# Performance work log

Hardware: AMD Instinct MI355X
Metric: run time of the kernel (lower is better)

Reference implementation:

```python
import jax, jax.numpy as jnp
import numpy as np
import math

D, NS, PP, POS = 256, 4, 4, 16
PI = math.pi
LN_EPS = 1e-5


def _gelu(x):
    return jax.nn.gelu(x, approximate=False)  # torch default GELU is exact erf


def _mlp(x, W1, b1, W2, b2):
    return _gelu(x @ W1 + b1) @ W2 + b2


def setup_inputs() -> dict:
    key = jax.random.key(0)
    ks = jax.random.split(key, 16)

    def lin(k, fi, fo):
        k1, k2 = jax.random.split(k)
        s = 1.0 / np.sqrt(fi)
        W = jax.random.uniform(k1, (fi, fo), minval=-s, maxval=s, dtype=jnp.float32)
        b = jax.random.uniform(k2, (fo,), minval=-s, maxval=s, dtype=jnp.float32)
        return W, b

    x = jax.random.normal(ks[0], (2, 2048, D), dtype=jnp.float32)
    kW1, kb1 = lin(ks[1], D, D); kW2, kb2 = lin(ks[2], D, NS * PP)
    qW1, qb1 = lin(ks[3], D, D); qW2, qb2 = lin(ks[4], D, NS * PP)
    vW, vb = lin(ks[5], D, D)
    oW, ob = lin(ks[6], D, D)
    gW1, gb1 = lin(ks[7], D, D // 2); gW2, gb2 = lin(ks[8], D // 2, 1)
    lW1, lb1 = lin(ks[9], D, D); lW2, lb2 = lin(ks[10], D, POS)
    lvW, lvb = lin(ks[11], D, D)
    pos_freqs = jnp.exp(jnp.arange(POS, dtype=jnp.float32) * (-math.log(10000.0) / POS))
    return dict(
        x=x, kW1=kW1, kb1=kb1, kW2=kW2, kb2=kb2,
        qW1=qW1, qb1=qb1, qW2=qW2, qb2=qb2, vW=vW, vb=vb,
        ln_g=jnp.ones((D,), jnp.float32), ln_b=jnp.zeros((D,), jnp.float32), oW=oW, ob=ob,
        set_weights=jnp.ones((NS,), jnp.float32), pos_freqs=pos_freqs,
        pos_weight=jnp.ones((1,), jnp.float32),
        gW1=gW1, gb1=gb1, gW2=gW2, gb2=gb2,
        lW1=lW1, lb1=lb1, lW2=lW2, lb2=lb2, lvW=lvW, lvb=lvb,
        surprise_scale=jnp.float32(1.0), surprise_bias=jnp.float32(0.0),
        ltm_weight=jnp.float32(0.5),
    )


def _fwd(x, kW1, kb1, kW2, kb2, qW1, qb1, qW2, qb2, vW, vb, ln_g, ln_b, oW, ob,
         set_weights, pos_freqs, pos_weight, gW1, gb1, gW2, gb2,
         lW1, lb1, lW2, lb2, lvW, lvb, surprise_scale, surprise_bias, ltm_weight):
    B, L, Dd = x.shape
    key_phasor = jnp.exp(1j * (jnp.tanh(_mlp(x, kW1, kb1, kW2, kb2)) * PI)).reshape(B, L, NS, PP)
    query_phasor = jnp.exp(1j * (jnp.tanh(_mlp(x, qW1, qb1, qW2, qb2)) * PI)).reshape(B, L, NS, PP)
    V_real = x @ vW + vb  # (B,L,D)
    weights = jax.nn.softmax(set_weights)

    pos_cb = jnp.maximum(jnp.arange(L, dtype=jnp.float32), 1.0)  # shifted positions, clamp(min=1)

    # ---- cross-bank (joint product over sets) + surprise write gate ----
    joint_key = jnp.prod(key_phasor, axis=2)    # (B,L,PP)
    joint_query = jnp.prod(query_phasor, axis=2)
    km_shift = jnp.concatenate(
        [jnp.zeros_like(joint_key[:, :1]), jnp.cumsum(joint_key[:, :-1], axis=1)], axis=1)
    res_mag = jnp.abs((km_shift * jnp.conj(joint_key)).sum(-1))  # (B,L)
    familiarity = jnp.clip(res_mag / (pos_cb * math.sqrt(PP)), 0.0, 1.0)[..., None]
    write_gate = jax.nn.sigmoid(surprise_scale * ((1.0 - familiarity) - 0.5) + surprise_bias)
    V_gated = (V_real * write_gate).astype(jnp.complex64)

    bound = joint_key[..., None] * V_gated[:, :, None, :]       # (B,L,PP,D)
    memory = jnp.cumsum(bound, axis=1)
    cross_bank = (memory * jnp.conj(joint_query)[..., None]).sum(2).real  # (B,L,D)

    # ---- per-bank binding/retrieval ----
    bound_all = key_phasor[..., None] * V_gated[:, :, None, None, :]  # (B,L,NS,PP,D)
    mem_all = jnp.cumsum(bound_all, axis=1)
    retr_per_bank = (mem_all * jnp.conj(query_phasor)[..., None]).sum(3).real  # (B,L,NS,D)
    total = (retr_per_bank * weights[None, None, :, None]).sum(2)
    total = (total + cross_bank) / (NS + 1)

    # ---- positional phasor bank ----
    V = V_real.astype(jnp.complex64)
    pos_phasor = jnp.exp(1j * (jnp.arange(L, dtype=jnp.float32)[:, None] * pos_freqs * 2 * PI))  # (L,POS)
    bound_pos = pos_phasor[None, :, :, None] * V[:, :, None, :]  # (B,L,POS,D)
    mem_pos = jnp.cumsum(bound_pos, axis=1)
    retr_pos = (mem_pos * jnp.conj(pos_phasor)[None, :, :, None]).sum(2).real
    gate = jax.nn.sigmoid(_mlp(x, gW1, gb1, gW2, gb2))  # (B,L,1)
    total = gate * total + (1 - gate) * (jax.nn.sigmoid(pos_weight) * retr_pos)

    # ---- LTM bank with surprise gating ----
    ltm_kp = jnp.exp(1j * (jnp.tanh(_mlp(x, lW1, lb1, lW2, lb2)) * PI))  # (B,L,POS)
    ltm_val = x @ lvW + lvb
    km2 = jnp.concatenate(
        [jnp.zeros_like(ltm_kp[:, :1]), jnp.cumsum(ltm_kp[:, :-1], axis=1)], axis=1)
    res2 = jnp.abs((km2 * jnp.conj(ltm_kp)).sum(-1))
    fam2 = jnp.clip(res2 / (pos_cb * math.sqrt(POS)), 0.0, 1.0)[..., None]
    wg2 = jax.nn.sigmoid(surprise_scale * ((1.0 - fam2) - 0.5) + surprise_bias)  # (B,L,1)
    gated_bind = wg2[:, :, None, :] * ltm_kp[..., None] * ltm_val.astype(jnp.complex64)[:, :, None, :]
    ltm_mem = jnp.cumsum(gated_bind, axis=1)                      # (B,L,POS,D)
    ltm_retr = (ltm_mem * jnp.conj(ltm_kp)[..., None]).sum(2).real
    pos1 = jnp.arange(1, L + 1, dtype=jnp.float32)
    ltm_retr = ltm_retr / jnp.sqrt(pos1 * POS)[None, :, None]
    total = total + jax.nn.sigmoid(ltm_weight) * ltm_retr

    # ---- output projection: LayerNorm + Linear, residual ----
    t = total / jnp.sqrt(pos1 * PP)[None, :, None]
    mu = t.mean(-1, keepdims=True)
    var = t.var(-1, keepdims=True)
    tn = (t - mu) / jnp.sqrt(var + LN_EPS) * ln_g + ln_b
    return x + tn @ oW + ob


def reference(x, kW1, kb1, kW2, kb2, qW1, qb1, qW2, qb2, vW, vb, ln_g, ln_b, oW, ob,
              set_weights, pos_freqs, pos_weight, gW1, gb1, gW2, gb2,
              lW1, lb1, lW2, lb2, lvW, lvb, surprise_scale, surprise_bias, ltm_weight):
    return _fwd(x, kW1, kb1, kW2, kb2, qW1, qb1, qW2, qb2, vW, vb, ln_g, ln_b, oW, ob,
                set_weights, pos_freqs, pos_weight, gW1, gb1, gW2, gb2,
                lW1, lb1, lW2, lb2, lvW, lvb, surprise_scale, surprise_bias, ltm_weight)
```

## Files before the change

### kernel.cpp

```cpp
#include <hip/hip_runtime.h>
#include <math.h>

#define DD   256
#define NSB  4
#define PPB  4
#define POSB 16
#define LL   2048
#define BB   2
#define NC   32
#define CHK  64
#define NG   13
#define FS   128
#define PI_F 3.14159265358979323846f

#define JK_OFF   0
#define JQ_OFF   8
#define KP_OFF   16
#define QP_OFF   48
#define LKP_OFF  80
#define GATE_OFF 112

#define FEAT_O  0L
#define V_O     524288L
#define LV_O    1572864L
#define PPH_O   2621440L
#define TOT_O   2686976L
#define CMEM_O  3735552L
#define WGB_O   5439488L
#define WS_FLOATS 5447680L
#define KM_O    CMEM_O
#define XH_O    CMEM_O
#define XL_O    (CMEM_O + 524288L)
#define WTH_O   (CMEM_O + 1048576L)
#define WT2H_O  (CMEM_O + 1245184L)

typedef __attribute__((ext_vector_type(8))) short bf16x8;
typedef __attribute__((ext_vector_type(4))) float f32x4;

__device__ __forceinline__ float sigm(float v){ return 1.0f/(1.0f+expf(-v)); }
__device__ __forceinline__ float gelu_exact(float v){ return 0.5f*v*(1.0f+erff(v*0.70710678118654752f)); }
__device__ __forceinline__ unsigned short f2bf(float f){
    unsigned u = __float_as_uint(f);
    unsigned r = u + 0x7fffu + ((u>>16)&1u);
    return (unsigned short)(r>>16);
}
__device__ __forceinline__ float bf2f(unsigned short h){ return __uint_as_float(((unsigned)h)<<16); }

__global__ __launch_bounds__(256) void prep_all(
    const float* __restrict__ x,
    const float* __restrict__ kW1, const float* __restrict__ qW1, const float* __restrict__ lW1,
    const float* __restrict__ vW,  const float* __restrict__ lvW, const float* __restrict__ gW1,
    const float* __restrict__ kW2, const float* __restrict__ qW2, const float* __restrict__ lW2,
    const float* __restrict__ pf,
    unsigned short* __restrict__ xh, unsigned short* __restrict__ xl,
    unsigned short* __restrict__ wth, unsigned short* __restrict__ wt2h,
    float* __restrict__ posph)
{
    int bid = blockIdx.x, tid = threadIdx.x;
    if (bid < 512){
        int gid = bid*256 + tid;
        int frag = gid>>6, lane = gid&63;
        int tile = frag>>3, ksb = frag&7;
        int row = tile*16 + (lane&15);
        int k0  = ksb*32 + ((lane>>4)&3)*8;
        const float* xp = x + (long)row*DD + k0;
        unsigned short h8[8], l8[8];
        #pragma unroll
        for (int e=0;e<8;++e){
            float f = xp[e];
            unsigned short h = f2bf(f);
            h8[e] = h;
            l8[e] = f2bf(f - bf2f(h));
        }
        *(bf16x8*)(xh + (long)gid*8) = *(bf16x8*)h8;
        *(bf16x8*)(xl + (long)gid*8) = *(bf16x8*)l8;
    } else if (bid < 512+192){
        int gid = (bid-512)*256 + tid;
        int frag = gid>>6, lane = gid&63;
        int tile = frag>>3, ksb = frag&7;
        int col = tile*16 + (lane&15);
        int k0  = ksb*32 + ((lane>>4)&3)*8;
        unsigned short h8[8];
        #pragma unroll
        for (int e=0;e<8;++e){
            int fi = k0 + e;
            float w = 0.f;
            if (col < 1408){
                int m = col >> 8;
                if (m < 5){
                    const float* W = (m==0)?kW1:((m==1)?qW1:((m==2)?lW1:((m==3)?vW:lvW)));
                    w = W[(long)fi*DD + (col & 255)];
                } else {
                    w = gW1[(long)fi*128 + (col - 1280)];
                }
            }
            h8[e] = f2bf(w);
        }
        *(bf16x8*)(wth + (long)gid*8) = *(bf16x8*)h8;
    } else if (bid < 512+192+48){
        int blk = bid - (512+192);
        int m = blk>>4, o = blk&15;
        const float* W2 = (m==0)?kW2:((m==1)?qW2:lW2);
        wt2h[(long)blk*DD + tid] = f2bf(W2[tid*16+o]);
    } else {
        int t = (bid - (512+192+48))*256 + tid;
        if (t < LL){
            #pragma unroll
            for (int j=0;j<POSB;++j){
                float ang = (((float)t * pf[j]) * 2.0f) * PI_F;
                float s,c; sincosf(ang,&s,&c);
                posph[t*32+2*j]   = c;
                posph[t*32+2*j+1] = s;
            }
        }
    }
}

__global__ __launch_bounds__(256) void mlp_fused(
    const unsigned short* __restrict__ xh, const unsigned short* __restrict__ xl,
    const unsigned short* __restrict__ wth, const unsigned short* __restrict__ wt2h,
    const float* __restrict__ kb1, const float* __restrict__ kb2,
    const float* __restrict__ qb1, const float* __restrict__ qb2,
    const float* __restrict__ lb1, const float* __restrict__ lb2,
    const float* __restrict__ vb,  const float* __restrict__ lvb,
    const float* __restrict__ gb1, const float* __restrict__ gW2, const float* __restrict__ gb2,
    float* __restrict__ feat, float* __restrict__ Vbuf, float* __restrict__ lvalbuf)
{
    __shared__ __align__(16) char smraw[18432];
    int tid = threadIdx.x, lane = tid & 63, wv = tid >> 6;
    int mat = blockIdx.x >> 7, bm = blockIdx.x & 127;
    int rowg0 = bm*32;
    int ar = lane & 15, kk = (lane>>4)*8;

    f32x4 acc[2][4];
    #pragma unroll
    for (int i=0;i<2;++i)
        #pragma unroll
        for (int j=0;j<4;++j) acc[i][j] = (f32x4){0.f,0.f,0.f,0.f};

    bf16x8 ah[2], al[2], bh[4];
    {
        #pragma unroll
        for (int i=0;i<2;++i){
            long off = (((long)(2*bm+i)*8 + 0)*64 + lane)*8;
            ah[i] = *reinterpret_cast<const bf16x8*>(xh + off);
            al[i] = *reinterpret_cast<const bf16x8*>(xl + off);
        }
        #pragma unroll
        for (int j=0;j<4;++j){
            long off = (((long)(mat*16 + wv*4 + j)*8 + 0)*64 + lane)*8;
            bh[j] = *reinterpret_cast<const bf16x8*>(wth + off);
        }
    }
    #pragma unroll
    for (int ksb=0; ksb<8; ++ksb){
        bf16x8 nah[2], nal[2], nbh[4];
        if (ksb < 7){
            #pragma unroll
            for (int i=0;i<2;++i){
                long off = (((long)(2*bm+i)*8 + ksb+1)*64 + lane)*8;
                nah[i] = *reinterpret_cast<const bf16x8*>(xh + off);
                nal[i] = *reinterpret_cast<const bf16x8*>(xl + off);
            }
            #pragma unroll
            for (int j=0;j<4;++j){
                long off = (((long)(mat*16 + wv*4 + j)*8 + ksb+1)*64 + lane)*8;
                nbh[j] = *reinterpret_cast<const bf16x8*>(wth + off);
            }
        }
        #pragma unroll
        for (int i=0;i<2;++i)
            #pragma unroll
            for (int j=0;j<4;++j){
                acc[i][j] = __builtin_amdgcn_mfma_f32_16x16x32_bf16(ah[i], bh[j], acc[i][j], 0,0,0);
                acc[i][j] = __builtin_amdgcn_mfma_f32_16x16x32_bf16(al[i], bh[j], acc[i][j], 0,0,0);
            }
        if (ksb < 7){
            #pragma unroll
            for (int i=0;i<2;++i){ ah[i]=nah[i]; al[i]=nal[i]; }
            #pragma unroll
            for (int j=0;j<4;++j) bh[j]=nbh[j];
        }
    }

    int rl0 = (lane>>4)*4;

    if (mat < 3){
        float (*ang)[16] = (float(*)[16])(smraw + 16384);
        const float* b1 = (mat==0)?kb1:((mat==1)?qb1:lb1);
        #pragma unroll
        for (int i=0;i<2;++i)
            #pragma unroll
            for (int j=0;j<4;++j){
                int c = wv*64 + j*16 + ar;
                #pragma unroll
                for (int r=0;r<4;++r){
                    int row = i*16 + rl0 + r;
                    float hv = gelu_exact(acc[i][j][r] + b1[c]);
                    int bo = row*512 + c*2;
                    *(unsigned short*)(smraw + (bo ^ ((row&7)<<4))) = f2bf(hv);
                }
            }
        __syncthreads();
        const float* b2 = (mat==0)?kb2:((mat==1)?qb2:lb2);
        int off = (mat==0)?KP_OFF:((mat==1)?QP_OFF:LKP_OFF);
        if (wv < 2){
            int arow = wv*16 + ar;
            f32x4 a2 = (f32x4){0.f,0.f,0.f,0.f};
            #pragma unroll
            for (int ksb=0; ksb<8; ++ksb){
                int k = ksb*32 + kk;
                int bo = arow*512 + k*2;
                bf16x8 af = *reinterpret_cast<const bf16x8*>(smraw + (bo ^ ((arow&7)<<4)));
                bf16x8 bf = *reinterpret_cast<const bf16x8*>(wt2h + ((long)(mat*16 + ar)*DD + k));
                a2 = __builtin_amdgcn_mfma_f32_16x16x32_bf16(af, bf, a2, 0,0,0);
            }
            int o = ar;
            #pragma unroll
            for (int r=0;r<4;++r){
                int tok = wv*16 + rl0 + r;
                float a = tanhf(a2[r] + b2[o])*PI_F;
                ang[tok][o] = a;
                float sn,cs; sincosf(a,&sn,&cs);
                long rowg = rowg0 + tok;
                feat[rowg*FS + off + 2*o]   = cs;
                feat[rowg*FS + off + 2*o+1] = sn;
            }
        }
        __syncthreads();
        if (mat<2 && tid<128){
            int tok = tid>>2, p = tid&3;
            float a = ang[tok][p]+ang[tok][4+p]+ang[tok][8+p]+ang[tok][12+p];
            float sn,cs; sincosf(a,&sn,&cs);
            int joff = (mat==0)?JK_OFF:JQ_OFF;
            long rowg = rowg0 + tok;
            feat[rowg*FS + joff + 2*p]   = cs;
            feat[rowg*FS + joff + 2*p+1] = sn;
        }
    } else if (mat < 5){
        const float* bv = (mat==3)? vb : lvb;
        float* dst = (mat==3)? Vbuf : lvalbuf;
        #pragma unroll
        for (int i=0;i<2;++i)
            #pragma unroll
            for (int j=0;j<4;++j){
                int c = wv*64 + j*16 + ar;
                #pragma unroll
                for (int r=0;r<4;++r)
                    dst[(long)(rowg0 + i*16 + rl0 + r)*DD + c] = acc[i][j][r] + bv[c];
            }
    } else {
        float (*hg)[132] = (float(*)[132])smraw;
        float (*part)[8] = (float(*)[8])(smraw + 32*132*4);
        if (wv < 2){
            #pragma unroll
            for (int i=0;i<2;++i)
                #pragma unroll
                for (int j=0;j<4;++j){
                    int c = wv*64 + j*16 + ar;
                    #pragma unroll
                    for (int r=0;r<4;++r)
                        hg[i*16 + rl0 + r][c] = gelu_exact(acc[i][j][r] + gb1[c]);
                }
        }
        __syncthreads();
        {
            int tok = tid>>3, jj = tid&7;
            float s = 0.f;
            #pragma unroll
            for (int c=0;c<16;++c) s += hg[tok][jj*16+c]*gW2[jj*16+c];
            part[tok][jj] = s;
        }
        __syncthreads();
        if (tid < 32){
            float s = gb2[0];
            #pragma unroll
            for (int j=0;j<8;++j) s += part[tid][j];
            feat[(long)(rowg0+tid)*FS + GATE_OFF] = sigm(s);
        }
    }
}

__global__ __launch_bounds__(256) void g_prefix(const float* __restrict__ feat, float* __restrict__ km){
    int b = blockIdx.x / 40, ch = blockIdx.x % 40;
    int off = (ch<8) ? (JK_OFF+ch) : (LKP_OFF + (ch-8));
    int tid = threadIdx.x;
    long rb = (long)b*LL*FS;
    float v[8]; float s = 0.f;
    #pragma unroll
    for (int u=0;u<8;++u){
        v[u] = feat[rb + (long)(tid*8+u)*FS + off];
        s += v[u];
    }
    int lane = tid & 63, w = tid >> 6;
    float xsc = s;
    #pragma unroll
    for (int o=1;o<64;o<<=1){ float y = __shfl_up(xsc,o); if (lane>=o) xsc += y; }
    __shared__ float wsum[4];
    if (lane==63) wsum[w] = xsc;
    __syncthreads();
    float woff = 0.f;
    for (int i=0;i<w;++i) woff += wsum[i];
    float run = (xsc - s) + woff;
    #pragma unroll
    for (int u=0;u<8;++u){
        km[((long)b*LL + tid*8+u)*40 + ch] = run;
        run += v[u];
    }
}

__global__ __launch_bounds__(256) void g_fam(
    const float* __restrict__ feat, const float* __restrict__ km,
    const float* __restrict__ ss_p, const float* __restrict__ sb_p,
    float* __restrict__ wgbuf)
{
    int t = blockIdx.x*256 + threadIdx.x;
    if (t >= BB*LL) return;
    int tc = t % LL;
    float ss = ss_p[0], sb = sb_p[0];
    long frow = (long)t*FS;
    const float* kmrow = km + (long)t*40;
    float pcb = fmaxf((float)tc, 1.0f);

    float sr=0.f, si=0.f;
    #pragma unroll
    for (int p=0;p<4;++p){
        float kr = feat[frow+JK_OFF+2*p], ki = feat[frow+JK_OFF+2*p+1];
        float kmr = kmrow[2*p], kmi = kmrow[2*p+1];
        sr += kmr*kr + kmi*ki;
        si += kmi*kr - kmr*ki;
    }
    float res = sqrtf(sr*sr+si*si);
    float fam = fminf(fmaxf(res/(pcb*2.0f),0.f),1.f);
    wgbuf[(long)t*2] = sigm(ss*(0.5f-fam)+sb);

    sr=0.f; si=0.f;
    #pragma unroll
    for (int p=0;p<16;++p){
        float kr = feat[frow+LKP_OFF+2*p], ki = feat[frow+LKP_OFF+2*p+1];
        float kmr = kmrow[8+2*p], kmi = kmrow[8+2*p+1];
        sr += kmr*kr + kmi*ki;
        si += kmi*kr - kmr*ki;
    }
    float res2 = sqrtf(sr*sr+si*si);
    float fam2 = fminf(fmaxf(res2/(pcb*4.0f),0.f),1.f);
    wgbuf[(long)t*2+1] = sigm(ss*(0.5f-fam2)+sb);
}

__global__ __launch_bounds__(128) void m_chunksum(
    const float* __restrict__ feat, const float* __restrict__ posph,
    const float* __restrict__ wgbuf, const float* __restrict__ Vbuf,
    const float* __restrict__ lvalbuf, float* __restrict__ cmem)
{
    int blk = blockIdx.x;
    int dh = blk & 1; blk >>= 1;
    int b = blk/(NG*NC); int r = blk%(NG*NC); int g = r/NC, c = r%NC;
    int d = dh*128 + threadIdx.x;
    __shared__ __align__(16) float4 kl4[CHK][2];
    __shared__ float gl[CHK];
    long frow = ((long)b*LL + c*CHK)*FS;
    for (int idx=threadIdx.x; idx<CHK*2; idx+=128){
        int t = idx>>1, j = idx&1;
        float4 v;
        if (g==0)       v = *(const float4*)&feat[frow + (long)t*FS + JK_OFF + j*4];
        else if (g<5)   v = *(const float4*)&feat[frow + (long)t*FS + KP_OFF + (g-1)*8 + j*4];
        else if (g<9)   v = *(const float4*)&posph[(long)(c*CHK+t)*32 + (g-5)*8 + j*4];
        else            v = *(const float4*)&feat[frow + (long)t*FS + LKP_OFF + (g-9)*8 + j*4];
        kl4[t][j] = v;
    }
    for (int t=threadIdx.x; t<CHK; t+=128){
        float gf;
        if (g<5)      gf = wgbuf[((long)b*LL + c*CHK + t)*2];
        else if (g<9) gf = 1.0f;
        else          gf = wgbuf[((long)b*LL + c*CHK + t)*2 + 1];
        gl[t] = gf;
    }
    __syncthreads();
    const float* vsrc = (g>=9)? lvalbuf : Vbuf;
    long vrow = ((long)b*LL + c*CHK)*DD + d;
    float m0r=0,m0i=0,m1r=0,m1i=0,m2r=0,m2i=0,m3r=0,m3i=0;
    float vnext = vsrc[vrow];
    #pragma unroll 4
    for (int t=0;t<CHK;++t){
        float v = vnext * gl[t];
        if (t+1 < CHK) vnext = vsrc[vrow + (long)(t+1)*DD];
        float4 ka = kl4[t][0], kb = kl4[t][1];
        m0r += ka.x*v; m0i += ka.y*v;
        m1r += ka.z*v; m1i += ka.w*v;
        m2r += kb.x*v; m2i += kb.y*v;
        m3r += kb.z*v; m3i += kb.w*v;
    }
    long grp = (long)((b*NG+g)*NC + c);
    long ob = grp*8*DD + d;
    cmem[ob+0*DD]=m0r; cmem[ob+1*DD]=m0i;
    cmem[ob+2*DD]=m1r; cmem[ob+3*DD]=m1i;
    cmem[ob+4*DD]=m2r; cmem[ob+5*DD]=m2i;
    cmem[ob+6*DD]=m3r; cmem[ob+7*DD]=m3i;
}

__global__ __launch_bounds__(256) void m_scan(float* __restrict__ cmem){
    int line = blockIdx.x;
    int lb = line>>2, slot = line&3, d = threadIdx.x;
    float vr[NC], vi[NC];
    #pragma unroll
    for (int c=0;c<NC;++c){
        long a = (((long)(lb*NC + c)*4 + slot)*2)*DD + d;
        vr[c] = cmem[a]; vi[c] = cmem[a+DD];
    }
    float rr=0.f, ri=0.f;
    #pragma unroll
    for (int c=0;c<NC;++c){
        long a = (((long)(lb*NC + c)*4 + slot)*2)*DD + d;
        cmem[a] = rr; cmem[a+DD] = ri;
        rr += vr[c]; ri += vi[c];
    }
}

__global__ __launch_bounds__(128) void m_retrieve_fam(
    const float* __restrict__ feat, const float* __restrict__ posph,
    const float* __restrict__ wgbuf, const float* __restrict__ Vbuf,
    const float* __restrict__ lvalbuf, const float* __restrict__ cmem,
    const float* __restrict__ set_w, const float* __restrict__ pos_w,
    const float* __restrict__ ltm_w, float* __restrict__ total)
{
    int blk = blockIdx.x;
    int dh = blk & 1; blk >>= 1;
    int b = blk/(3*NC); int r = blk%(3*NC); int fam = r/NC, c = r%NC;
    int d = dh*128 + threadIdx.x;
    __shared__ __align__(16) float4 s_k04[CHK][4];
    __shared__ __align__(16) float4 s_kb4[CHK][8];
    __shared__ __align__(16) float4 s_qb4[CHK][8];
    __shared__ float s_sc[CHK][2];
    long frow = ((long)b*LL + c*CHK)*FS;

    for (int idx=threadIdx.x; idx<CHK*8; idx+=128){
        int t = idx>>3, j = idx&7;
        if (fam==0){
            s_kb4[t][j] = *(const float4*)&feat[frow + (long)t*FS + KP_OFF + j*4];
            s_qb4[t][j] = *(const float4*)&feat[frow + (long)t*FS + QP_OFF + j*4];
        } else if (fam==1){
            s_kb4[t][j] = *(const float4*)&posph[(long)(c*CHK+t)*32 + j*4];
        } else {
            s_kb4[t][j] = *(const float4*)&feat[frow + (long)t*FS + LKP_OFF + j*4];
        }
    }
    if (fam==0){
        for (int idx=threadIdx.x; idx<CHK*4; idx+=128){
            int t = idx>>2, j = idx&3;
            s_k04[t][j] = *(const float4*)&feat[frow + (long)t*FS + JK_OFF + j*4];
        }
    }
    for (int t=threadIdx.x; t<CHK; t+=128){
        int tc = c*CHK + t;
        float gate = feat[frow + (long)t*FS + GATE_OFF];
        if (fam==0){
            s_sc[t][0] = wgbuf[((long)b*LL+tc)*2];
            s_sc[t][1] = gate*0.2f;
        } else if (fam==1){
            s_sc[t][0] = (1.0f-gate)*sigm(pos_w[0]);
            s_sc[t][1] = 0.f;
        } else {
            s_sc[t][0] = wgbuf[((long)b*LL+tc)*2+1];
            s_sc[t][1] = sigm(ltm_w[0]) * rsqrtf((float)(tc+1)*16.0f);
        }
    }
    __syncthreads();

    long vrow = ((long)b*LL + c*CHK)*DD + d;
    float* tp = total + ((long)b*LL + c*CHK)*DD + d;

    if (fam == 0){
        float w0=expf(set_w[0]),w1=expf(set_w[1]),w2=expf(set_w[2]),w3=expf(set_w[3]);
        float den = w0+w1+w2+w3;
        float wn[4] = {w0/den, w1/den, w2/den, w3/den};
        float cr[4], ci[4], br[4][4], bi[4][4];
        #pragma unroll
        for (int s=0;s<4;++s){
            long cb0 = (((long)(b*NG+0)*NC + c)*8 + 2*s)*DD + d;
            cr[s] = cmem[cb0]; ci[s] = cmem[cb0+DD];
        }
        #pragma unroll
        for (int g=0;g<4;++g)
            #pragma unroll
            for (int s=0;s<4;++s){
                long cb = (((long)(b*NG+1+g)*NC + c)*8 + 2*s)*DD + d;
                br[g][s] = cmem[cb]; bi[g][s] = cmem[cb+DD];
            }
        float vnext = Vbuf[vrow];
        #pragma unroll 2
        for (int t=0;t<CHK;++t){
            float v = vnext;
            if (t+1 < CHK) vnext = Vbuf[vrow + (long)(t+1)*DD];
            float vg = v * s_sc[t][0];
            float4 jk0 = s_k04[t][0], jk1 = s_k04[t][1];
            float4 jq0 = s_k04[t][2], jq1 = s_k04[t][3];
            cr[0] += jk0.x*vg; ci[0] += jk0.y*vg;
            cr[1] += jk0.z*vg; ci[1] += jk0.w*vg;
            cr[2] += jk1.x*vg; ci[2] += jk1.y*vg;
            cr[3] += jk1.z*vg; ci[3] += jk1.w*vg;
            float rsc = cr[0]*jq0.x + ci[0]*jq0.y + cr[1]*jq0.z + ci[1]*jq0.w
                      + cr[2]*jq1.x + ci[2]*jq1.y + cr[3]*jq1.z + ci[3]*jq1.w;
            float rbank = 0.f;
            #pragma unroll
            for (int g=0;g<4;++g){
                float4 ka = s_kb4[t][2*g], kb = s_kb4[t][2*g+1];
                float4 qa = s_qb4[t][2*g], qb = s_qb4[t][2*g+1];
                br[g][0] += ka.x*vg; bi[g][0] += ka.y*vg;
                br[g][1] += ka.z*vg; bi[g][1] += ka.w*vg;
                br[g][2] += kb.x*vg; bi[g][2] += kb.y*vg;
                br[g][3] += kb.z*vg; bi[g][3] += kb.w*vg;
                float rg = br[g][0]*qa.x + bi[g][0]*qa.y + br[g][1]*qa.z + bi[g][1]*qa.w
                         + br[g][2]*qb.x + bi[g][2]*qb.y + br[g][3]*qb.z + bi[g][3]*qb.w;
                rbank += rg*wn[g];
            }
            float rs = s_sc[t][1]*(rsc + rbank);
            atomicAdd(tp + (long)t*DD, rs);
        }
    } else {
        const float* vsrc = (fam==2)? lvalbuf : Vbuf;
        int g0 = (fam==1)? 5 : 9;
        float mr[16], mi[16];
        #pragma unroll
        for (int g=0;g<4;++g)
            #pragma unroll
            for (int s=0;s<4;++s){
                long cb = (((long)(b*NG+g0+g)*NC + c)*8 + 2*s)*DD + d;
                mr[g*4+s] = cmem[cb]; mi[g*4+s] = cmem[cb+DD];
            }
        float vnext = vsrc[vrow];
        #pragma unroll 2
        for (int t=0;t<CHK;++t){
            float v = vnext;
            if (t+1 < CHK) vnext = vsrc[vrow + (long)(t+1)*DD];
            float vg = (fam==2)? v*s_sc[t][0] : v;
            float rs = 0.f;
            #pragma unroll
            for (int j=0;j<8;++j){
                float4 ka = s_kb4[t][j];
                mr[2*j]   += ka.x*vg; mi[2*j]   += ka.y*vg;
                rs += mr[2*j]*ka.x + mi[2*j]*ka.y;
                mr[2*j+1] += ka.z*vg; mi[2*j+1] += ka.w*vg;
                rs += mr[2*j+1]*ka.z + mi[2*j+1]*ka.w;
            }
            float sc = (fam==2)? s_sc[t][1] : s_sc[t][0];
            atomicAdd(tp + (long)t*DD, rs*sc);
        }
    }
}

__global__ __launch_bounds__(256) void k4_out(
    const float* __restrict__ x, const float* __restrict__ total,
    const float* __restrict__ ln_g, const float* __restrict__ ln_b,
    const float* __restrict__ oW,  const float* __restrict__ obv,
    float* __restrict__ out)
{
    __shared__ float tn[8][DD];
    int tid = threadIdx.x;
    long base = (long)blockIdx.x*8;
    int wave = tid>>6, lane = tid&63;
    for (int wtok=0; wtok<2; ++wtok){
        int tok = wave*2 + wtok;
        long row = base + tok;
        int tc = (int)(row % LL);
        float inv = rsqrtf((float)(tc+1)*4.0f);
        float4 tv4 = ((const float4*)(total + row*DD))[lane];
        float vals[4] = {tv4.x*inv, tv4.y*inv, tv4.z*inv, tv4.w*inv};
        float s=0.f, s2=0.f;
        #pragma unroll
        for (int k=0;k<4;++k){ s += vals[k]; s2 += vals[k]*vals[k]; }
        for (int o=1;o<64;o<<=1){ s += __shfl_xor(s,o); s2 += __shfl_xor(s2,o); }
        float mu = s/256.f, var = s2/256.f - mu*mu;
        float rstd = rsqrtf(var + 1e-5f);
        float4 w;
        w.x = (vals[0]-mu)*rstd*ln_g[lane*4+0] + ln_b[lane*4+0];
        w.y = (vals[1]-mu)*rstd*ln_g[lane*4+1] + ln_b[lane*4+1];
        w.z = (vals[2]-mu)*rstd*ln_g[lane*4+2] + ln_b[lane*4+2];
        w.w = (vals[3]-mu)*rstd*ln_g[lane*4+3] + ln_b[lane*4+3];
        ((float4*)&tn[tok][0])[lane] = w;
    }
    __syncthreads();
    float acc[8];
    #pragma unroll
    for (int tok=0;tok<8;++tok) acc[tok]=obv[tid];
    #pragma unroll 4
    for (int i=0;i<DD;++i){
        float w = oW[i*DD+tid];
        #pragma unroll
        for (int tok=0;tok<8;++tok) acc[tok] += tn[tok][i]*w;
    }
    for (int tok=0;tok<8;++tok){
        long row = base+tok;
        out[row*DD+tid] = x[row*DD+tid] + acc[tok];
    }
}

extern "C" void kernel_launch(void* const* d_in, const int* in_sizes, int n_in,
                              void* d_out, int out_size, void* d_ws, size_t ws_size,
                              hipStream_t stream)
{
    const float* x    = (const float*)d_in[0];
    const float* kW1  = (const float*)d_in[1];
    const float* kb1  = (const float*)d_in[2];
    const float* kW2  = (const float*)d_in[3];
    const float* kb2  = (const float*)d_in[4];
    const float* qW1  = (const float*)d_in[5];
    const float* qb1  = (const float*)d_in[6];
    const float* qW2  = (const float*)d_in[7];
    const float* qb2  = (const float*)d_in[8];
    const float* vW   = (const float*)d_in[9];
    const float* vb   = (const float*)d_in[10];
    const float* ln_g = (const float*)d_in[11];
    const float* ln_b = (const float*)d_in[12];
    const float* oW   = (const float*)d_in[13];
    const float* ob   = (const float*)d_in[14];
    const float* set_w= (const float*)d_in[15];
    const float* pf   = (const float*)d_in[16];
    const float* pw   = (const float*)d_in[17];
    const float* gW1  = (const float*)d_in[18];
    const float* gb1  = (const float*)d_in[19];
    const float* gW2  = (const float*)d_in[20];
    const float* gb2  = (const float*)d_in[21];
    const float* lW1  = (const float*)d_in[22];
    const float* lb1  = (const float*)d_in[23];
    const float* lW2  = (const float*)d_in[24];
    const float* lb2  = (const float*)d_in[25];
    const float* lvW  = (const float*)d_in[26];
    const float* lvb  = (const float*)d_in[27];
    const float* ss   = (const float*)d_in[28];
    const float* sb   = (const float*)d_in[29];
    const float* lw   = (const float*)d_in[30];
    float* out = (float*)d_out;

    float* ws    = (float*)d_ws;
    float* feat  = ws + FEAT_O;
    float* Vbuf  = ws + V_O;
    float* lval  = ws + LV_O;
    float* posph = ws + PPH_O;
    float* total = ws + TOT_O;
    float* cmem  = ws + CMEM_O;
    float* km    = ws + KM_O;
    float* wgbuf = ws + WGB_O;
    unsigned short* xh   = (unsigned short*)(ws + XH_O);
    unsigned short* xl   = (unsigned short*)(ws + XL_O);
    unsigned short* wth  = (unsigned short*)(ws + WTH_O);
    unsigned short* wt2h = (unsigned short*)(ws + WT2H_O);

    (void)in_sizes; (void)n_in; (void)out_size; (void)ws_size;

    hipMemsetAsync(total, 0, (size_t)BB*LL*DD*sizeof(float), stream);

    prep_all <<<512+192+48+8, 256, 0, stream>>>(x, kW1,qW1,lW1,vW,lvW,gW1, kW2,qW2,lW2,
                                                pf, xh, xl, wth, wt2h, posph);
    mlp_fused<<<6*128, 256, 0, stream>>>(xh,xl,wth,wt2h,
                                         kb1,kb2, qb1,qb2, lb1,lb2,
                                         vb,lvb, gb1,gW2,gb2, feat, Vbuf, lval);
    g_prefix <<<BB*40, 256, 0, stream>>>(feat, km);
    g_fam    <<<(BB*LL+255)/256, 256, 0, stream>>>(feat, km, ss, sb, wgbuf);
    m_chunksum <<<BB*NG*NC*2, 128, 0, stream>>>(feat, posph, wgbuf, Vbuf, lval, cmem);
    m_scan     <<<BB*NG*4, 256, 0, stream>>>(cmem);
    m_retrieve_fam <<<BB*3*NC*2, 128, 0, stream>>>(feat, posph, wgbuf, Vbuf, lval, cmem,
                                                   set_w, pw, lw, total);
    k4_out     <<<BB*LL/8, 256, 0, stream>>>(x, total, ln_g, ln_b, oW, ob, out);
}
```

Before: 118.0 us.

## Halve chunk size, merge pos/LTM retrieval, replace atomics with two output buffers

```diff
diff --git a/kernel.cpp b/kernel.cpp
--- a/kernel.cpp
+++ b/kernel.cpp
@@ -7,8 +7,8 @@
 #define POSB 16
 #define LL   2048
 #define BB   2
-#define NC   32
-#define CHK  64
+#define NC   64
+#define CHK  32
 #define NG   13
 #define FS   128
 #define PI_F 3.14159265358979323846f
@@ -26,8 +26,9 @@
 #define PPH_O   2621440L
 #define TOT_O   2686976L
 #define CMEM_O  3735552L
-#define WGB_O   5439488L
-#define WS_FLOATS 5447680L
+#define WGB_O   7143424L
+#define TOT2_O  7151616L
+#define WS_FLOATS 8200192L
 #define KM_O    CMEM_O
 #define XH_O    CMEM_O
 #define XL_O    (CMEM_O + 524288L)
@@ -400,76 +401,75 @@
 
 __global__ __launch_bounds__(256) void m_scan(float* __restrict__ cmem){
     int line = blockIdx.x;
-    int lb = line>>2, slot = line&3, d = threadIdx.x;
-    float vr[NC], vi[NC];
+    int comp = line & 1; int l2 = line >> 1;
+    int lb = l2>>2, slot = l2&3, d = threadIdx.x;
+    float v[NC];
     #pragma unroll
     for (int c=0;c<NC;++c){
-        long a = (((long)(lb*NC + c)*4 + slot)*2)*DD + d;
-        vr[c] = cmem[a]; vi[c] = cmem[a+DD];
-    }
-    float rr=0.f, ri=0.f;
+        long a = ((((long)(lb*NC + c)*4 + slot)*2) + comp)*DD + d;
+        v[c] = cmem[a];
+    }
+    float run = 0.f;
     #pragma unroll
     for (int c=0;c<NC;++c){
-        long a = (((long)(lb*NC + c)*4 + slot)*2)*DD + d;
-        cmem[a] = rr; cmem[a+DD] = ri;
-        rr += vr[c]; ri += vi[c];
-    }
-}
-
-__global__ __launch_bounds__(128) void m_retrieve_fam(
+        long a = ((((long)(lb*NC + c)*4 + slot)*2) + comp)*DD + d;
+        cmem[a] = run;
+        run += v[c];
+    }
+}
+
+__global__ __launch_bounds__(128) void m_retrieve2(
     const float* __restrict__ feat, const float* __restrict__ posph,
     const float* __restrict__ wgbuf, const float* __restrict__ Vbuf,
     const float* __restrict__ lvalbuf, const float* __restrict__ cmem,
     const float* __restrict__ set_w, const float* __restrict__ pos_w,
-    const float* __restrict__ ltm_w, float* __restrict__ total)
+    const float* __restrict__ ltm_w, float* __restrict__ totA, float* __restrict__ totB)
 {
     int blk = blockIdx.x;
+    int half = blk & 1; blk >>= 1;
     int dh = blk & 1; blk >>= 1;
-    int b = blk/(3*NC); int r = blk%(3*NC); int fam = r/NC, c = r%NC;
+    int c = blk % NC; int b = blk / NC;
     int d = dh*128 + threadIdx.x;
-    __shared__ __align__(16) float4 s_k04[CHK][4];
-    __shared__ __align__(16) float4 s_kb4[CHK][8];
-    __shared__ __align__(16) float4 s_qb4[CHK][8];
-    __shared__ float s_sc[CHK][2];
+    __shared__ __align__(16) float4 sA[CHK][8];
+    __shared__ __align__(16) float4 sB[CHK][8];
+    __shared__ __align__(16) float4 sC[CHK][4];
+    __shared__ float sSc[CHK][3];
     long frow = ((long)b*LL + c*CHK)*FS;
 
     for (int idx=threadIdx.x; idx<CHK*8; idx+=128){
         int t = idx>>3, j = idx&7;
-        if (fam==0){
-            s_kb4[t][j] = *(const float4*)&feat[frow + (long)t*FS + KP_OFF + j*4];
-            s_qb4[t][j] = *(const float4*)&feat[frow + (long)t*FS + QP_OFF + j*4];
-        } else if (fam==1){
-            s_kb4[t][j] = *(const float4*)&posph[(long)(c*CHK+t)*32 + j*4];
+        if (half==0){
+            sA[t][j] = *(const float4*)&feat[frow + (long)t*FS + KP_OFF + j*4];
+            sB[t][j] = *(const float4*)&feat[frow + (long)t*FS + QP_OFF + j*4];
         } else {
-            s_kb4[t][j] = *(const float4*)&feat[frow + (long)t*FS + LKP_OFF + j*4];
-        }
-    }
-    if (fam==0){
+            sA[t][j] = *(const float4*)&posph[(long)(c*CHK+t)*32 + j*4];
+            sB[t][j] = *(const float4*)&feat[frow + (long)t*FS + LKP_OFF + j*4];
+        }
+    }
+    if (half==0){
         for (int idx=threadIdx.x; idx<CHK*4; idx+=128){
             int t = idx>>2, j = idx&3;
-            s_k04[t][j] = *(const float4*)&feat[frow + (long)t*FS + JK_OFF + j*4];
+            sC[t][j] = *(const float4*)&feat[frow + (long)t*FS + JK_OFF + j*4];
         }
     }
     for (int t=threadIdx.x; t<CHK; t+=128){
         int tc = c*CHK + t;
         float gate = feat[frow + (long)t*FS + GATE_OFF];
-        if (fam==0){
-            s_sc[t][0] = wgbuf[((long)b*LL+tc)*2];
-            s_sc[t][1] = gate*0.2f;
-        } else if (fam==1){
-            s_sc[t][0] = (1.0f-gate)*sigm(pos_w[0]);
-            s_sc[t][1] = 0.f;
+        if (half==0){
+            sSc[t][0] = wgbuf[((long)b*LL+tc)*2];
+            sSc[t][1] = gate*0.2f;
         } else {
-            s_sc[t][0] = wgbuf[((long)b*LL+tc)*2+1];
-            s_sc[t][1] = sigm(ltm_w[0]) * rsqrtf((float)(tc+1)*16.0f);
+            sSc[t][0] = (1.0f-gate)*sigm(pos_w[0]);
+            sSc[t][1] = wgbuf[((long)b*LL+tc)*2+1];
+            sSc[t][2] = sigm(ltm_w[0]) * rsqrtf((float)(tc+1)*16.0f);
         }
     }
     __syncthreads();
 
     long vrow = ((long)b*LL + c*CHK)*DD + d;
-    float* tp = total + ((long)b*LL + c*CHK)*DD + d;
-
-    if (fam == 0){
+
+    if (half == 0){
+        float* tp = totA + ((long)b*LL + c*CHK)*DD + d;
         float w0=expf(set_w[0]),w1=expf(set_w[1]),w2=expf(set_w[2]),w3=expf(set_w[3]);
         float den = w0+w1+w2+w3;
         float wn[4] = {w0/den, w1/den, w2/den, w3/den};
@@ -491,9 +491,9 @@
         for (int t=0;t<CHK;++t){
             float v = vnext;
             if (t+1 < CHK) vnext = Vbuf[vrow + (long)(t+1)*DD];
-            float vg = v * s_sc[t][0];
-            float4 jk0 = s_k04[t][0], jk1 = s_k04[t][1];
-            float4 jq0 = s_k04[t][2], jq1 = s_k04[t][3];
+            float vg = v * sSc[t][0];
+            float4 jk0 = sC[t][0], jk1 = sC[t][1];
+            float4 jq0 = sC[t][2], jq1 = sC[t][3];
             cr[0] += jk0.x*vg; ci[0] += jk0.y*vg;
             cr[1] += jk0.z*vg; ci[1] += jk0.w*vg;
             cr[2] += jk1.x*vg; ci[2] += jk1.y*vg;
@@ -503,8 +503,8 @@
             float rbank = 0.f;
             #pragma unroll
             for (int g=0;g<4;++g){
-                float4 ka = s_kb4[t][2*g], kb = s_kb4[t][2*g+1];
-                float4 qa = s_qb4[t][2*g], qb = s_qb4[t][2*g+1];
+                float4 ka = sA[t][2*g], kb = sA[t][2*g+1];
+                float4 qa = sB[t][2*g], qb = sB[t][2*g+1];
                 br[g][0] += ka.x*vg; bi[g][0] += ka.y*vg;
                 br[g][1] += ka.z*vg; bi[g][1] += ka.w*vg;
                 br[g][2] += kb.x*vg; bi[g][2] += kb.y*vg;
@@ -513,43 +513,52 @@
                          + br[g][2]*qb.x + bi[g][2]*qb.y + br[g][3]*qb.z + bi[g][3]*qb.w;
                 rbank += rg*wn[g];
             }
-            float rs = s_sc[t][1]*(rsc + rbank);
-            atomicAdd(tp + (long)t*DD, rs);
+            tp[(long)t*DD] = sSc[t][1]*(rsc + rbank);
         }
     } else {
-        const float* vsrc = (fam==2)? lvalbuf : Vbuf;
-        int g0 = (fam==1)? 5 : 9;
-        float mr[16], mi[16];
+        float* tp = totB + ((long)b*LL + c*CHK)*DD + d;
+        float pr[16], pi2[16], lr[16], li[16];
         #pragma unroll
         for (int g=0;g<4;++g)
             #pragma unroll
             for (int s=0;s<4;++s){
-                long cb = (((long)(b*NG+g0+g)*NC + c)*8 + 2*s)*DD + d;
-                mr[g*4+s] = cmem[cb]; mi[g*4+s] = cmem[cb+DD];
-            }
-        float vnext = vsrc[vrow];
+                long cb = (((long)(b*NG+5+g)*NC + c)*8 + 2*s)*DD + d;
+                pr[g*4+s] = cmem[cb]; pi2[g*4+s] = cmem[cb+DD];
+                long cb2 = (((long)(b*NG+9+g)*NC + c)*8 + 2*s)*DD + d;
+                lr[g*4+s] = cmem[cb2]; li[g*4+s] = cmem[cb2+DD];
+            }
+        float vnext = Vbuf[vrow];
+        float lvnext = lvalbuf[vrow];
         #pragma unroll 2
         for (int t=0;t<CHK;++t){
-            float v = vnext;
-            if (t+1 < CHK) vnext = vsrc[vrow + (long)(t+1)*DD];
-            float vg = (fam==2)? v*s_sc[t][0] : v;
-            float rs = 0.f;
+            float v = vnext, lv = lvnext;
+            if (t+1 < CHK){
+                vnext = Vbuf[vrow + (long)(t+1)*DD];
+                lvnext = lvalbuf[vrow + (long)(t+1)*DD];
+            }
+            float vgl = lv * sSc[t][1];
+            float rpos = 0.f, rltm = 0.f;
             #pragma unroll
             for (int j=0;j<8;++j){
-                float4 ka = s_kb4[t][j];
-                mr[2*j]   += ka.x*vg; mi[2*j]   += ka.y*vg;
-                rs += mr[2*j]*ka.x + mi[2*j]*ka.y;
-                mr[2*j+1] += ka.z*vg; mi[2*j+1] += ka.w*vg;
-                rs += mr[2*j+1]*ka.z + mi[2*j+1]*ka.w;
-            }
-            float sc = (fam==2)? s_sc[t][1] : s_sc[t][0];
-            atomicAdd(tp + (long)t*DD, rs*sc);
+                float4 pa = sA[t][j];
+                pr[2*j]   += pa.x*v; pi2[2*j]   += pa.y*v;
+                rpos += pr[2*j]*pa.x + pi2[2*j]*pa.y;
+                pr[2*j+1] += pa.z*v; pi2[2*j+1] += pa.w*v;
+                rpos += pr[2*j+1]*pa.z + pi2[2*j+1]*pa.w;
+                float4 la = sB[t][j];
+                lr[2*j]   += la.x*vgl; li[2*j]   += la.y*vgl;
+                rltm += lr[2*j]*la.x + li[2*j]*la.y;
+                lr[2*j+1] += la.z*vgl; li[2*j+1] += la.w*vgl;
+                rltm += lr[2*j+1]*la.z + li[2*j+1]*la.w;
+            }
+            tp[(long)t*DD] = sSc[t][0]*rpos + sSc[t][2]*rltm;
         }
     }
 }
 
 __global__ __launch_bounds__(256) void k4_out(
-    const float* __restrict__ x, const float* __restrict__ total,
+    const float* __restrict__ x, const float* __restrict__ totA,
+    const float* __restrict__ totB,
     const float* __restrict__ ln_g, const float* __restrict__ ln_b,
     const float* __restrict__ oW,  const float* __restrict__ obv,
     float* __restrict__ out)
@@ -563,8 +572,9 @@
         long row = base + tok;
         int tc = (int)(row % LL);
         float inv = rsqrtf((float)(tc+1)*4.0f);
-        float4 tv4 = ((const float4*)(total + row*DD))[lane];
-        float vals[4] = {tv4.x*inv, tv4.y*inv, tv4.z*inv, tv4.w*inv};
+        float4 ta = ((const float4*)(totA + row*DD))[lane];
+        float4 tb = ((const float4*)(totB + row*DD))[lane];
+        float vals[4] = {(ta.x+tb.x)*inv, (ta.y+tb.y)*inv, (ta.z+tb.z)*inv, (ta.w+tb.w)*inv};
         float s=0.f, s2=0.f;
         #pragma unroll
         for (int k=0;k<4;++k){ s += vals[k]; s2 += vals[k]*vals[k]; }
@@ -640,14 +650,13 @@
     float* cmem  = ws + CMEM_O;
     float* km    = ws + KM_O;
     float* wgbuf = ws + WGB_O;
+    float* tot2  = ws + TOT2_O;
     unsigned short* xh   = (unsigned short*)(ws + XH_O);
     unsigned short* xl   = (unsigned short*)(ws + XL_O);
     unsigned short* wth  = (unsigned short*)(ws + WTH_O);
     unsigned short* wt2h = (unsigned short*)(ws + WT2H_O);
 
     (void)in_sizes; (void)n_in; (void)out_size; (void)ws_size;
-
-    hipMemsetAsync(total, 0, (size_t)BB*LL*DD*sizeof(float), stream);
 
     prep_all <<<512+192+48+8, 256, 0, stream>>>(x, kW1,qW1,lW1,vW,lvW,gW1, kW2,qW2,lW2,
                                                 pf, xh, xl, wth, wt2h, posph);
@@ -657,8 +666,8 @@
     g_prefix <<<BB*40, 256, 0, stream>>>(feat, km);
     g_fam    <<<(BB*LL+255)/256, 256, 0, stream>>>(feat, km, ss, sb, wgbuf);
     m_chunksum <<<BB*NG*NC*2, 128, 0, stream>>>(feat, posph, wgbuf, Vbuf, lval, cmem);
-    m_scan     <<<BB*NG*4, 256, 0, stream>>>(cmem);
-    m_retrieve_fam <<<BB*3*NC*2, 128, 0, stream>>>(feat, posph, wgbuf, Vbuf, lval, cmem,
-                                                   set_w, pw, lw, total);
-    k4_out     <<<BB*LL/8, 256, 0, stream>>>(x, total, ln_g, ln_b, oW, ob, out);
-}
+    m_scan     <<<BB*NG*4*2, 256, 0, stream>>>(cmem);
+    m_retrieve2 <<<BB*NC*2*2, 128, 0, stream>>>(feat, posph, wgbuf, Vbuf, lval, cmem,
+                                                set_w, pw, lw, total, tot2);
+    k4_out     <<<BB*LL/8, 256, 0, stream>>>(x, total, tot2, ln_g, ln_b, oW, ob, out);
+}
```

After: 109.0 us. 1.08x faster.
